# Performance work log

Measured on AMD Instinct MI355X. Metric: run time of the kernel, lower is better.

## Reference

```python
import jax, jax.numpy as jnp
import numpy as np

N_NODES = 100000

def _sage_conv(x, src, dst, deg_inv, Wl, bl, Wr):
    # PyG SAGEConv (aggr='mean', root_weight=True):
    #   out = lin_l(mean_{j in N(i)} x_j) + lin_r(x_i)
    msg = x[src]                                            # [E, d]
    agg = jax.ops.segment_sum(msg, dst, num_segments=N_NODES)  # [N, d]
    agg = agg * deg_inv                                     # mean (0 for isolated nodes)
    return agg @ Wl.T + bl + x @ Wr.T


def setup_inputs() -> dict:
    key = jax.random.key(0)
    ks = jax.random.split(key, 12)
    N, E, d_in, d_h, d_out = N_NODES, 1600000, 64, 64, 32
    x = jax.random.normal(ks[0], (N, d_in), dtype=jnp.float32)
    edge_index = jax.random.randint(ks[1], (2, E), 0, N, dtype=jnp.int64)

    def glorot(k, shape):
        fan_in = shape[1]
        return jax.random.normal(k, shape, dtype=jnp.float32) / np.sqrt(fan_in)

    return {
        "x": x,
        "edge_index": edge_index,
        "W1l": glorot(ks[2], (d_h, d_in)), "b1l": jnp.zeros((d_h,), jnp.float32), "W1r": glorot(ks[3], (d_h, d_in)),
        "W2l": glorot(ks[4], (d_h, d_h)),  "b2l": jnp.zeros((d_h,), jnp.float32), "W2r": glorot(ks[5], (d_h, d_h)),
        "W3l": glorot(ks[6], (d_h, d_h)),  "b3l": jnp.zeros((d_h,), jnp.float32), "W3r": glorot(ks[7], (d_h, d_h)),
        "Wfc": glorot(ks[8], (d_out, d_h)), "bfc": jnp.zeros((d_out,), jnp.float32),
    }


def reference(x, edge_index, W1l, b1l, W1r, W2l, b2l, W2r, W3l, b3l, W3r, Wfc, bfc):
    src, dst = edge_index[0], edge_index[1]
    # in-degree per destination node (shared by all three conv layers)
    ones = jnp.ones((src.shape[0],), x.dtype)
    deg = jax.ops.segment_sum(ones, dst, num_segments=N_NODES)
    deg_inv = (1.0 / jnp.maximum(deg, 1.0))[:, None]        # [N, 1]

    h = jax.nn.relu(_sage_conv(x, src, dst, deg_inv, W1l, b1l, W1r))
    # dropout(p=0.5) is identity in eval mode
    h = jax.nn.relu(_sage_conv(h, src, dst, deg_inv, W2l, b2l, W2r))
    h = jax.nn.relu(_sage_conv(h, src, dst, deg_inv, W3l, b3l, W3r))
    return h @ Wfc.T + bfc
```

## Files before the change

### kernel.cpp

```cpp
#include <hip/hip_runtime.h>
#include <hip/hip_fp16.h>

#define N_NODES 100000
#define D 64
#define BR 256
#define NB 391
#define ECH 2560
#define NROWPAD 100096
#define CSRCAP 6144

typedef _Float16 f16x8 __attribute__((ext_vector_type(8)));
typedef float f32x4 __attribute__((ext_vector_type(4)));

__device__ __forceinline__ float rlf(float v, int l) {
    union { float f; int i; } u;
    u.f = v;
    u.i = __builtin_amdgcn_readlane(u.i, l);
    return u.f;
}

__global__ __launch_bounds__(256) void k_prep(const float* __restrict__ Wl1, const float* __restrict__ Wr1,
                                              const float* __restrict__ Wl2, const float* __restrict__ Wr2,
                                              const float* __restrict__ Wl3, const float* __restrict__ Wr3,
                                              const float* __restrict__ Wfc,
                                              __half* __restrict__ Wf1, __half* __restrict__ Wf2,
                                              __half* __restrict__ Wf3, __half* __restrict__ Wffc,
                                              unsigned* __restrict__ x16, unsigned* __restrict__ H1,
                                              unsigned* __restrict__ H2,
                                              int* __restrict__ histT, int entries, int ntail,
                                              const float4* __restrict__ x, int n4) {
    int t = blockIdx.x * 256 + threadIdx.x;
    if (t >= 65536) {
        int i = t - 65536;
        if (i < n4) {
            float4 v = x[i];
            union { __half2 h[2]; uint2 u; } pk;
            pk.h[0] = __floats2half2_rn(v.x, v.y);
            pk.h[1] = __floats2half2_rn(v.z, v.w);
            ((uint2*)x16)[i] = pk.u;
        }
    } else if (t < 24576) {
        int layer = t / 8192;
        int r = t % 8192;
        int f = r >> 9, rem = r & 511;
        int lane = rem >> 3, i = rem & 7;
        int kt = f >> 2, nt = f & 3;
        int k = kt * 32 + (lane >> 4) * 8 + i;
        int o = nt * 16 + (lane & 15);
        const float* Wl = layer == 0 ? Wl1 : layer == 1 ? Wl2 : Wl3;
        const float* Wr = layer == 0 ? Wr1 : layer == 1 ? Wr2 : Wr3;
        float v = (k < 64) ? Wl[o * 64 + k] : Wr[o * 64 + (k - 64)];
        __half* Wf = layer == 0 ? Wf1 : layer == 1 ? Wf2 : Wf3;
        Wf[r] = __float2half(v);
    } else if (t < 26624) {
        int r = t - 24576;
        int f = r >> 9, rem = r & 511;
        int lane = rem >> 3, i = rem & 7;
        int kt = f >> 1, nt = f & 1;
        int k = kt * 32 + (lane >> 4) * 8 + i;
        int o = nt * 16 + (lane & 15);
        Wffc[r] = __float2half(Wfc[o * 64 + k]);
    } else if (t < 26720) {
        int z = t - 26624;
        unsigned* buf = (z >> 5) == 0 ? x16 : (z >> 5) == 1 ? H1 : H2;
        buf[(size_t)N_NODES * 32 + (z & 31)] = 0u;
    } else if (t >= 32768 && t < 32768 + ntail) {
        histT[entries + (t - 32768)] = 0;
    }
}


__global__ __launch_bounds__(512) void k_hist(const int* __restrict__ dst,
                                              int* __restrict__ histT,
                                              int E, int ga) {
    __shared__ int h[NB];
    int blk = blockIdx.x, tid = threadIdx.x;
    for (int i = tid; i < NB; i += 512) h[i] = 0;
    __syncthreads();
    int base = blk * ECH;
    int lim = E - base; if (lim > ECH) lim = ECH;
    for (int i = tid; i < lim; i += 512)
        atomicAdd(&h[dst[base + i] >> 8], 1);
    __syncthreads();
    for (int i = tid; i < NB; i += 512)
        histT[i * ga + blk] = h[i];
}

__global__ __launch_bounds__(256) void k_scan1(const int* __restrict__ cnt,
                                               int* __restrict__ part,
                                               int* __restrict__ bsums) {
    __shared__ int s[256];
    int tid = threadIdx.x;
    int i4 = blockIdx.x * 256 + tid;
    int4 v = reinterpret_cast<const int4*>(cnt)[i4];
    int tsum = v.x + v.y + v.z + v.w;
    s[tid] = tsum;
    __syncthreads();
    for (int off = 1; off < 256; off <<= 1) {
        int t = 0;
        if (tid >= off) t = s[tid - off];
        __syncthreads();
        if (tid >= off) s[tid] += t;
        __syncthreads();
    }
    int excl = tid ? s[tid - 1] : 0;
    if (tid == 255) bsums[blockIdx.x] = s[255];
    int4 o;
    o.x = excl;
    o.y = o.x + v.x;
    o.z = o.y + v.y;
    o.w = o.z + v.z;
    reinterpret_cast<int4*>(part)[i4] = o;
}

__global__ __launch_bounds__(256) void k_scan2(int* __restrict__ bsums, int nb,
                                               int* __restrict__ col) {
    __shared__ int s[256];
    int tid = threadIdx.x;
    if (tid < 8) col[tid] = N_NODES;
    int v = (tid < nb) ? bsums[tid] : 0;
    s[tid] = v;
    __syncthreads();
    for (int off = 1; off < 256; off <<= 1) {
        int t = 0;
        if (tid >= off) t = s[tid - off];
        __syncthreads();
        if (tid >= off) s[tid] += t;
        __syncthreads();
    }
    if (tid < nb) bsums[tid] = tid ? s[tid - 1] : 0;
}

__global__ __launch_bounds__(512) void k_part(const int* __restrict__ src,
                                              const int* __restrict__ dst,
                                              const int* __restrict__ offs,
                                              const int* __restrict__ bsums,
                                              int* __restrict__ bedge,
                                              int E, int ga) {
    __shared__ int o[NB];
    int blk = blockIdx.x, tid = threadIdx.x;
    for (int i = tid; i < NB; i += 512) {
        int ent = i * ga + blk;
        o[i] = offs[ent] + bsums[ent >> 10];
    }
    __syncthreads();
    int base = blk * ECH;
    int lim = E - base; if (lim > ECH) lim = ECH;
    for (int i = tid; i < lim; i += 512) {
        int e = base + i;
        int d = dst[e];
        int pos = atomicAdd(&o[d >> 8], 1);
        bedge[pos] = src[e] | ((d & 255) << 17);
    }
}

__global__ __launch_bounds__(512) void k_csr(const int* __restrict__ bedge,
                                             const int* __restrict__ offs,
                                             const int* __restrict__ bsums,
                                             int* __restrict__ col,
                                             int2* __restrict__ rp,
                                             float* __restrict__ deg_inv,
                                             int E, int ga) {
    __shared__ int ebuf[CSRCAP];
    __shared__ int lcnt[BR];
    __shared__ int stmp[BR];
    __shared__ int lcur[BR];
    int b = blockIdx.x, tid = threadIdx.x;
    int e0 = b * ga;
    int ebeg = offs[e0] + bsums[e0 >> 10];
    int eend = E;
    if (b + 1 < NB) {
        int e1 = (b + 1) * ga;
        eend = offs[e1] + bsums[e1 >> 10];
    }
    int cnt = eend - ebeg;
    int nbase = b * BR;
    int cbase = ebeg + b * (BR * 4) + 8;
    if (tid < 256) lcnt[tid] = 0;
    __syncthreads();
    for (int i = tid; i < cnt; i += 512) {
        int ed = bedge[ebeg + i];
        if (i < CSRCAP) ebuf[i] = ed;
        atomicAdd(&lcnt[ed >> 17], 1);
    }
    __syncthreads();
    int v = 0, pdeg = 0;
    if (tid < 256) {
        v = lcnt[tid];
        pdeg = (v + 3) & ~3;
        stmp[tid] = pdeg;
    }
    __syncthreads();
    for (int off = 1; off < 256; off <<= 1) {
        int t = 0;
        if (tid < 256 && tid >= off) t = stmp[tid - off];
        __syncthreads();
        if (tid < 256 && tid >= off) stmp[tid] += t;
        __syncthreads();
    }
    if (tid < 256) {
        int ex = tid ? stmp[tid - 1] : 0;
        int slot = cbase + ex;
        lcur[tid] = slot;
        int node = nbase + tid;
        if (node < N_NODES) {
            rp[node] = make_int2(slot, slot + pdeg);
            deg_inv[node] = 1.0f / (float)(v > 1 ? v : 1);
            for (int s2 = slot + v; s2 < slot + pdeg; ++s2) col[s2] = N_NODES;
        }
    }
    __syncthreads();
    for (int i = tid; i < cnt; i += 512) {
        int ed = (i < CSRCAP) ? ebuf[i] : bedge[ebeg + i];
        int pos = atomicAdd(&lcur[ed >> 17], 1);
        col[pos] = ed & 0x1FFFF;
    }
}


__device__ __forceinline__ void fused_core(const __half* __restrict__ Hin,
                                           const __half* __restrict__ Wf,
                                           const float* __restrict__ bias,
                                           const int2* __restrict__ rp,
                                           const int* __restrict__ col,
                                           const float* __restrict__ deg_inv, int n,
                                           __half (&lds)[16][72], int m0, int l,
                                           f32x4 (&acc)[4]) {
    int q = l >> 4, li = l & 15;
    int beg = 0, nq = 0;
    float dinv = 0.f;
    if (l < 16 && m0 + l < n) {
        int2 se = rp[m0 + l];
        beg = se.x;
        nq = (se.y - se.x) >> 2;
        dinv = deg_inv[m0 + l];
    }
    const uint2* x8 = (const uint2*)Hin;
    const int* cq = col + q;

#pragma unroll
    for (int g = 0; g < 4; ++g) {
        int b0 = __builtin_amdgcn_readlane(beg, 4 * g + 0);
        int b1 = __builtin_amdgcn_readlane(beg, 4 * g + 1);
        int b2 = __builtin_amdgcn_readlane(beg, 4 * g + 2);
        int b3 = __builtin_amdgcn_readlane(beg, 4 * g + 3);
        int c0 = __builtin_amdgcn_readlane(nq, 4 * g + 0);
        int c1 = __builtin_amdgcn_readlane(nq, 4 * g + 1);
        int c2 = __builtin_amdgcn_readlane(nq, 4 * g + 2);
        int c3 = __builtin_amdgcn_readlane(nq, 4 * g + 3);
        int qmax = max(max(c0, c1), max(c2, c3));
        __half2 s00 = __floats2half2_rn(0.f, 0.f), s01 = s00;
        __half2 s10 = s00, s11 = s00, s20 = s00, s21 = s00, s30 = s00, s31 = s00;
        for (int qq = 0; qq < qmax; qq += 4) {
            int a[16];
#pragma unroll
            for (int s = 0; s < 4; ++s) {
                int o = (qq + s) * 4;
                a[s * 4 + 0] = qq + s < c0 ? b0 + o : 0;
                a[s * 4 + 1] = qq + s < c1 ? b1 + o : 0;
                a[s * 4 + 2] = qq + s < c2 ? b2 + o : 0;
                a[s * 4 + 3] = qq + s < c3 ? b3 + o : 0;
            }
            int idx[16];
#pragma unroll
            for (int i = 0; i < 16; ++i) idx[i] = cq[a[i]];
            uint2 u[16];
#pragma unroll
            for (int i = 0; i < 16; ++i) u[i] = x8[(size_t)idx[i] * 16 + li];
            union { unsigned v; __half2 h; } w;
#pragma unroll
            for (int s = 0; s < 4; ++s) {
                w.v = u[s * 4 + 0].x; s00 = __hadd2(s00, w.h);
                w.v = u[s * 4 + 0].y; s01 = __hadd2(s01, w.h);
                w.v = u[s * 4 + 1].x; s10 = __hadd2(s10, w.h);
                w.v = u[s * 4 + 1].y; s11 = __hadd2(s11, w.h);
                w.v = u[s * 4 + 2].x; s20 = __hadd2(s20, w.h);
                w.v = u[s * 4 + 2].y; s21 = __hadd2(s21, w.h);
                w.v = u[s * 4 + 3].x; s30 = __hadd2(s30, w.h);
                w.v = u[s * 4 + 3].y; s31 = __hadd2(s31, w.h);
            }
        }
        union { __half2 h; int i; } t;
#pragma unroll
        for (int m = 16; m < 64; m <<= 1) {
            t.h = s00; t.i = __shfl_xor(t.i, m); s00 = __hadd2(s00, t.h);
            t.h = s01; t.i = __shfl_xor(t.i, m); s01 = __hadd2(s01, t.h);
            t.h = s10; t.i = __shfl_xor(t.i, m); s10 = __hadd2(s10, t.h);
            t.h = s11; t.i = __shfl_xor(t.i, m); s11 = __hadd2(s11, t.h);
            t.h = s20; t.i = __shfl_xor(t.i, m); s20 = __hadd2(s20, t.h);
            t.h = s21; t.i = __shfl_xor(t.i, m); s21 = __hadd2(s21, t.h);
            t.h = s30; t.i = __shfl_xor(t.i, m); s30 = __hadd2(s30, t.h);
            t.h = s31; t.i = __shfl_xor(t.i, m); s31 = __hadd2(s31, t.h);
        }
        float d0 = rlf(dinv, 4 * g + 0);
        float d1 = rlf(dinv, 4 * g + 1);
        float d2 = rlf(dinv, 4 * g + 2);
        float d3 = rlf(dinv, 4 * g + 3);
        if (l < 16) {
            union { __half2 h; unsigned v; } p0, p1;
            float2 f;
            uint2 ov;
            f = __half22float2(s00); p0.h = __floats2half2_rn(f.x * d0, f.y * d0);
            f = __half22float2(s01); p1.h = __floats2half2_rn(f.x * d0, f.y * d0);
            ov.x = p0.v; ov.y = p1.v;
            *(uint2*)&lds[4 * g + 0][li * 4] = ov;
            f = __half22float2(s10); p0.h = __floats2half2_rn(f.x * d1, f.y * d1);
            f = __half22float2(s11); p1.h = __floats2half2_rn(f.x * d1, f.y * d1);
            ov.x = p0.v; ov.y = p1.v;
            *(uint2*)&lds[4 * g + 1][li * 4] = ov;
            f = __half22float2(s20); p0.h = __floats2half2_rn(f.x * d2, f.y * d2);
            f = __half22float2(s21); p1.h = __floats2half2_rn(f.x * d2, f.y * d2);
            ov.x = p0.v; ov.y = p1.v;
            *(uint2*)&lds[4 * g + 2][li * 4] = ov;
            f = __half22float2(s30); p0.h = __floats2half2_rn(f.x * d3, f.y * d3);
            f = __half22float2(s31); p1.h = __floats2half2_rn(f.x * d3, f.y * d3);
            ov.x = p0.v; ov.y = p1.v;
            *(uint2*)&lds[4 * g + 3][li * 4] = ov;
        }
    }

    const f16x8* wf8 = (const f16x8*)Wf;
    f16x8 bf[4][4];
#pragma unroll
    for (int kt = 0; kt < 4; ++kt)
#pragma unroll
        for (int nt = 0; nt < 4; ++nt)
            bf[kt][nt] = wf8[(kt * 4 + nt) * 64 + l];
    int rowA = li;
#pragma unroll
    for (int nt = 0; nt < 4; ++nt) {
        float bs = bias[nt * 16 + rowA];
        acc[nt] = (f32x4){bs, bs, bs, bs};
    }
#pragma unroll
    for (int kt = 0; kt < 4; ++kt) {
        f16x8 a;
        if (kt < 2)
            a = *(const f16x8*)&lds[rowA][kt * 32 + q * 8];
        else
            a = *(const f16x8*)(Hin + (size_t)(m0 + rowA) * D + (kt - 2) * 32 + q * 8);
#pragma unroll
        for (int nt = 0; nt < 4; ++nt)
            acc[nt] = __builtin_amdgcn_mfma_f32_16x16x32_f16(a, bf[kt][nt], acc[nt], 0, 0, 0);
    }
}

__global__ __launch_bounds__(256) void k_fused(const __half* __restrict__ Hin,
                                               __half* __restrict__ Hout,
                                               const __half* __restrict__ Wf,
                                               const float* __restrict__ bias,
                                               const int2* __restrict__ rp,
                                               const int* __restrict__ col,
                                               const float* __restrict__ deg_inv, int n) {
    __shared__ __half lds[4][16][72];
    int l = threadIdx.x & 63;
    int wv = threadIdx.x >> 6;
    int m0 = blockIdx.x * 64 + wv * 16;
    f32x4 acc[4];
    fused_core(Hin, Wf, bias, rp, col, deg_inv, n, lds[wv], m0, l, acc);
    int q = l >> 4, rowA = l & 15;
#pragma unroll
    for (int nt = 0; nt < 4; ++nt)
#pragma unroll
        for (int qd = 0; qd < 4; ++qd) {
            int node = m0 + q * 4 + qd;
            float v = fmaxf(acc[nt][qd], 0.f);
            if (node < n)
                Hout[(size_t)node * D + nt * 16 + rowA] = __float2half(v);
        }
}

__global__ __launch_bounds__(256) void k_fused_fc(const __half* __restrict__ Hin,
                                                  float* __restrict__ out,
                                                  const __half* __restrict__ Wf,
                                                  const float* __restrict__ bias,
                                                  const __half* __restrict__ Wffc,
                                                  const float* __restrict__ bfc,
                                                  const int2* __restrict__ rp,
                                                  const int* __restrict__ col,
                                                  const float* __restrict__ deg_inv, int n) {
    __shared__ __half lds[4][16][72];
    int l = threadIdx.x & 63;
    int wv = threadIdx.x >> 6;
    int m0 = blockIdx.x * 64 + wv * 16;
    f32x4 acc[4];
    fused_core(Hin, Wf, bias, rp, col, deg_inv, n, lds[wv], m0, l, acc);
    int q = l >> 4, li = l & 15;

#pragma unroll
    for (int nt = 0; nt < 4; ++nt)
#pragma unroll
        for (int qd = 0; qd < 4; ++qd)
            lds[wv][q * 4 + qd][nt * 16 + li] = __float2half(fmaxf(acc[nt][qd], 0.f));

    const f16x8* wfc8 = (const f16x8*)Wffc;
    f16x8 bf2[2][2];
#pragma unroll
    for (int kt = 0; kt < 2; ++kt)
#pragma unroll
        for (int nt = 0; nt < 2; ++nt)
            bf2[kt][nt] = wfc8[(kt * 2 + nt) * 64 + l];
    f32x4 acc2[2];
#pragma unroll
    for (int nt = 0; nt < 2; ++nt) {
        float bs = bfc[nt * 16 + li];
        acc2[nt] = (f32x4){bs, bs, bs, bs};
    }
#pragma unroll
    for (int kt = 0; kt < 2; ++kt) {
        f16x8 a = *(const f16x8*)&lds[wv][li][kt * 32 + q * 8];
#pragma unroll
        for (int nt = 0; nt < 2; ++nt)
            acc2[nt] = __builtin_amdgcn_mfma_f32_16x16x32_f16(a, bf2[kt][nt], acc2[nt], 0, 0, 0);
    }
#pragma unroll
    for (int nt = 0; nt < 2; ++nt)
#pragma unroll
        for (int qd = 0; qd < 4; ++qd) {
            int node = m0 + q * 4 + qd;
            if (node < n)
                out[(size_t)node * 32 + nt * 16 + li] = acc2[nt][qd];
        }
}


extern "C" void kernel_launch(void* const* d_in, const int* in_sizes, int n_in,
                              void* d_out, int out_size, void* d_ws, size_t ws_size,
                              hipStream_t stream) {
    const float* x   = (const float*)d_in[0];
    const int*   ei  = (const int*)d_in[1];
    const int    E   = in_sizes[1] / 2;
    const int*   src = ei;
    const int*   dst = ei + E;
    const float* W1l = (const float*)d_in[2];
    const float* b1l = (const float*)d_in[3];
    const float* W1r = (const float*)d_in[4];
    const float* W2l = (const float*)d_in[5];
    const float* b2l = (const float*)d_in[6];
    const float* W2r = (const float*)d_in[7];
    const float* W3l = (const float*)d_in[8];
    const float* b3l = (const float*)d_in[9];
    const float* W3r = (const float*)d_in[10];
    const float* Wfc = (const float*)d_in[11];
    const float* bfc = (const float*)d_in[12];
    float* out = (float*)d_out;

    const int ga      = (E + ECH - 1) / ECH;
    const int entries = NB * ga;
    const int padded  = (entries + 1023) & ~1023;
    const int ntail   = padded - entries;
    const int nb2     = padded / 1024;

    char* p = (char*)d_ws;
    size_t off = 0;
    auto take = [&](size_t bytes) -> void* {
        void* r = p + off;
        off = (off + bytes + 255) & ~(size_t)255;
        return r;
    };
    __half* x16    = (__half*)take((size_t)NROWPAD * D * 2);
    __half* H1     = (__half*)take((size_t)NROWPAD * D * 2);
    __half* H2     = (__half*)take((size_t)NROWPAD * D * 2);
    float* deg_inv = (float*)take((size_t)N_NODES * 4);
    int2*  rp      = (int2*)take((size_t)N_NODES * 8);
    int*   histT   = (int*)take((size_t)padded * 4);
    int*   offs    = (int*)take((size_t)padded * 4);
    int*   bsums   = (int*)take(256 * 4);
    int*   bedge   = (int*)take((size_t)E * 4);
    int*   col     = (int*)take((size_t)(E + NB * BR * 4 + 72) * 4);
    __half* Wf1    = (__half*)take(8192 * 2);
    __half* Wf2    = (__half*)take(8192 * 2);
    __half* Wf3    = (__half*)take(8192 * 2);
    __half* Wffc   = (__half*)take(2048 * 2);

    int n4 = N_NODES * D / 4;
    int gp = (65536 + n4 + 255) / 256;
    k_prep<<<gp, 256, 0, stream>>>(W1l, W1r, W2l, W2r, W3l, W3r, Wfc,
                                   Wf1, Wf2, Wf3, Wffc,
                                   (unsigned*)x16, (unsigned*)H1, (unsigned*)H2,
                                   histT, entries, ntail, (const float4*)x, n4);

    k_hist<<<ga, 512, 0, stream>>>(dst, histT, E, ga);
    k_scan1<<<nb2, 256, 0, stream>>>(histT, offs, bsums);
    k_scan2<<<1, 256, 0, stream>>>(bsums, nb2, col);
    k_part<<<ga, 512, 0, stream>>>(src, dst, offs, bsums, bedge, E, ga);
    k_csr<<<NB, 512, 0, stream>>>(bedge, offs, bsums, col, rp, deg_inv, E, ga);

    int gg = NROWPAD / 64;

    k_fused<<<gg, 256, 0, stream>>>(x16, H1, Wf1, b1l, rp, col, deg_inv, N_NODES);
    k_fused<<<gg, 256, 0, stream>>>(H1, H2, Wf2, b2l, rp, col, deg_inv, N_NODES);
    k_fused_fc<<<gg, 256, 0, stream>>>(H2, out, Wf3, b3l, Wffc, bfc, rp, col, deg_inv, N_NODES);
}
```

Baseline: 182.8 us.

## Split features into column slices and separate aggregation from GEMM

Feature matrices move to a sliced layout: four 16-column fp16 slices, each stored contiguously across all nodes. Aggregation becomes its own kernel that gathers one slice at a time, aiming for better cache locality of random gathers since each slice is a quarter of the full matrix. A separate MFMA GEMM kernel then reads the aggregated and root slices. This doubles the kernel launches and adds a round trip of the aggregate buffer through global memory.

Measured after the change: 420.2 us. 130% more time.

```diff
diff --git a/kernel.cpp b/kernel.cpp
--- a/kernel.cpp
+++ b/kernel.cpp
@@ -7,17 +7,10 @@
 #define NB 391
 #define ECH 2560
 #define NROWPAD 100096
-#define CSRCAP 6144
+#define SS ((size_t)NROWPAD * 16)
 
 typedef _Float16 f16x8 __attribute__((ext_vector_type(8)));
 typedef float f32x4 __attribute__((ext_vector_type(4)));
-
-__device__ __forceinline__ float rlf(float v, int l) {
-    union { float f; int i; } u;
-    u.f = v;
-    u.i = __builtin_amdgcn_readlane(u.i, l);
-    return u.f;
-}
 
 __global__ __launch_bounds__(256) void k_prep(const float* __restrict__ Wl1, const float* __restrict__ Wr1,
                                               const float* __restrict__ Wl2, const float* __restrict__ Wr2,
@@ -25,19 +18,27 @@
                                               const float* __restrict__ Wfc,
                                               __half* __restrict__ Wf1, __half* __restrict__ Wf2,
                                               __half* __restrict__ Wf3, __half* __restrict__ Wffc,
-                                              unsigned* __restrict__ x16, unsigned* __restrict__ H1,
-                                              unsigned* __restrict__ H2,
+                                              __half* __restrict__ x16, __half* __restrict__ H1,
+                                              __half* __restrict__ H2,
                                               int* __restrict__ histT, int entries, int ntail,
-                                              const float4* __restrict__ x, int n4) {
+                                              const float* __restrict__ x, int ncv) {
     int t = blockIdx.x * 256 + threadIdx.x;
     if (t >= 65536) {
         int i = t - 65536;
-        if (i < n4) {
-            float4 v = x[i];
-            union { __half2 h[2]; uint2 u; } pk;
-            pk.h[0] = __floats2half2_rn(v.x, v.y);
-            pk.h[1] = __floats2half2_rn(v.z, v.w);
-            ((uint2*)x16)[i] = pk.u;
+        if (i < ncv) {
+            int nd = i >> 2, p = i & 3;
+            const float4* xp = (const float4*)x + (size_t)nd * 16 + p * 4;
+            float4 v0 = xp[0], v1 = xp[1], v2 = xp[2], v3 = xp[3];
+            union { __half2 h; unsigned u; } a, b;
+            __half* d = x16 + (size_t)p * SS + (size_t)nd * 16;
+            a.h = __floats2half2_rn(v0.x, v0.y); b.h = __floats2half2_rn(v0.z, v0.w);
+            ((uint2*)d)[0] = make_uint2(a.u, b.u);
+            a.h = __floats2half2_rn(v1.x, v1.y); b.h = __floats2half2_rn(v1.z, v1.w);
+            ((uint2*)d)[1] = make_uint2(a.u, b.u);
+            a.h = __floats2half2_rn(v2.x, v2.y); b.h = __floats2half2_rn(v2.z, v2.w);
+            ((uint2*)d)[2] = make_uint2(a.u, b.u);
+            a.h = __floats2half2_rn(v3.x, v3.y); b.h = __floats2half2_rn(v3.z, v3.w);
+            ((uint2*)d)[3] = make_uint2(a.u, b.u);
         }
     } else if (t < 24576) {
         int layer = t / 8192;
@@ -62,8 +63,10 @@
         Wffc[r] = __float2half(Wfc[o * 64 + k]);
     } else if (t < 26720) {
         int z = t - 26624;
-        unsigned* buf = (z >> 5) == 0 ? x16 : (z >> 5) == 1 ? H1 : H2;
-        buf[(size_t)N_NODES * 32 + (z & 31)] = 0u;
+        int bsel = z >> 5, rem = z & 31;
+        int s = rem >> 3, u = rem & 7;
+        __half* buf = bsel == 0 ? x16 : bsel == 1 ? H1 : H2;
+        ((unsigned*)buf)[(size_t)s * (SS / 2) + (size_t)N_NODES * 8 + u] = 0u;
     } else if (t >= 32768 && t < 32768 + ntail) {
         histT[entries + (t - 32768)] = 0;
     }
@@ -117,7 +120,7 @@
                                                int* __restrict__ col) {
     __shared__ int s[256];
     int tid = threadIdx.x;
-    if (tid < 8) col[tid] = N_NODES;
+    if (tid < 16) col[tid] = N_NODES;
     int v = (tid < nb) ? bsums[tid] : 0;
     s[tid] = v;
     __syncthreads();
@@ -154,6 +157,7 @@
     }
 }
 
+#define CSRCAP 6144
 __global__ __launch_bounds__(512) void k_csr(const int* __restrict__ bedge,
                                              const int* __restrict__ offs,
                                              const int* __restrict__ bsums,
@@ -175,7 +179,7 @@
     }
     int cnt = eend - ebeg;
     int nbase = b * BR;
-    int cbase = ebeg + b * (BR * 4) + 8;
+    int cbase = ebeg + b * (BR * 4) + 16;
     if (tid < 256) lcnt[tid] = 0;
     __syncthreads();
     for (int i = tid; i < cnt; i += 512) {
@@ -218,107 +222,66 @@
 }
 
 
-__device__ __forceinline__ void fused_core(const __half* __restrict__ Hin,
-                                           const __half* __restrict__ Wf,
-                                           const float* __restrict__ bias,
-                                           const int2* __restrict__ rp,
-                                           const int* __restrict__ col,
-                                           const float* __restrict__ deg_inv, int n,
-                                           __half (&lds)[16][72], int m0, int l,
-                                           f32x4 (&acc)[4]) {
-    int q = l >> 4, li = l & 15;
-    int beg = 0, nq = 0;
-    float dinv = 0.f;
-    if (l < 16 && m0 + l < n) {
-        int2 se = rp[m0 + l];
-        beg = se.x;
-        nq = (se.y - se.x) >> 2;
-        dinv = deg_inv[m0 + l];
-    }
-    const uint2* x8 = (const uint2*)Hin;
-    const int* cq = col + q;
-
-#pragma unroll
-    for (int g = 0; g < 4; ++g) {
-        int b0 = __builtin_amdgcn_readlane(beg, 4 * g + 0);
-        int b1 = __builtin_amdgcn_readlane(beg, 4 * g + 1);
-        int b2 = __builtin_amdgcn_readlane(beg, 4 * g + 2);
-        int b3 = __builtin_amdgcn_readlane(beg, 4 * g + 3);
-        int c0 = __builtin_amdgcn_readlane(nq, 4 * g + 0);
-        int c1 = __builtin_amdgcn_readlane(nq, 4 * g + 1);
-        int c2 = __builtin_amdgcn_readlane(nq, 4 * g + 2);
-        int c3 = __builtin_amdgcn_readlane(nq, 4 * g + 3);
-        int qmax = max(max(c0, c1), max(c2, c3));
-        __half2 s00 = __floats2half2_rn(0.f, 0.f), s01 = s00;
-        __half2 s10 = s00, s11 = s00, s20 = s00, s21 = s00, s30 = s00, s31 = s00;
-        for (int qq = 0; qq < qmax; qq += 4) {
-            int a[16];
-#pragma unroll
-            for (int s = 0; s < 4; ++s) {
-                int o = (qq + s) * 4;
-                a[s * 4 + 0] = qq + s < c0 ? b0 + o : 0;
-                a[s * 4 + 1] = qq + s < c1 ? b1 + o : 0;
-                a[s * 4 + 2] = qq + s < c2 ? b2 + o : 0;
-                a[s * 4 + 3] = qq + s < c3 ? b3 + o : 0;
-            }
-            int idx[16];
-#pragma unroll
-            for (int i = 0; i < 16; ++i) idx[i] = cq[a[i]];
-            uint2 u[16];
-#pragma unroll
-            for (int i = 0; i < 16; ++i) u[i] = x8[(size_t)idx[i] * 16 + li];
+__global__ __launch_bounds__(256) void k_aggslice(const __half* __restrict__ Hin,
+                                                  __half* __restrict__ Agg,
+                                                  const int2* __restrict__ rp,
+                                                  const int* __restrict__ col,
+                                                  const float* __restrict__ deg_inv,
+                                                  int bps, int n) {
+    int slice = blockIdx.x / bps;
+    int blk = blockIdx.x % bps;
+    int l = threadIdx.x & 63;
+    int wv = threadIdx.x >> 6;
+    int e4 = l >> 2, c = l & 3;
+    int nbase = (blk * 4 + wv) * 16;
+    const __half* src = Hin + (size_t)slice * SS;
+    __half* dst = Agg + (size_t)slice * SS;
+    for (int i = 0; i < 16; ++i) {
+        int node = nbase + i;
+        if (node >= n) break;
+        int2 se = rp[node];
+        int beg = __builtin_amdgcn_readfirstlane(se.x);
+        int pdeg = __builtin_amdgcn_readfirstlane(se.y) - beg;
+        __half2 a0 = __floats2half2_rn(0.f, 0.f), a1 = a0;
+        for (int base = 0; base < pdeg; base += 16) {
+            int e = base + e4;
+            int addr = e < pdeg ? beg + e : e4;
+            int idx = col[addr];
+            uint2 u = *(const uint2*)(src + (size_t)idx * 16 + c * 4);
             union { unsigned v; __half2 h; } w;
-#pragma unroll
-            for (int s = 0; s < 4; ++s) {
-                w.v = u[s * 4 + 0].x; s00 = __hadd2(s00, w.h);
-                w.v = u[s * 4 + 0].y; s01 = __hadd2(s01, w.h);
-                w.v = u[s * 4 + 1].x; s10 = __hadd2(s10, w.h);
-                w.v = u[s * 4 + 1].y; s11 = __hadd2(s11, w.h);
-                w.v = u[s * 4 + 2].x; s20 = __hadd2(s20, w.h);
-                w.v = u[s * 4 + 2].y; s21 = __hadd2(s21, w.h);
-                w.v = u[s * 4 + 3].x; s30 = __hadd2(s30, w.h);
-                w.v = u[s * 4 + 3].y; s31 = __hadd2(s31, w.h);
-            }
-        }
-        union { __half2 h; int i; } t;
-#pragma unroll
-        for (int m = 16; m < 64; m <<= 1) {
-            t.h = s00; t.i = __shfl_xor(t.i, m); s00 = __hadd2(s00, t.h);
-            t.h = s01; t.i = __shfl_xor(t.i, m); s01 = __hadd2(s01, t.h);
-            t.h = s10; t.i = __shfl_xor(t.i, m); s10 = __hadd2(s10, t.h);
-            t.h = s11; t.i = __shfl_xor(t.i, m); s11 = __hadd2(s11, t.h);
-            t.h = s20; t.i = __shfl_xor(t.i, m); s20 = __hadd2(s20, t.h);
-            t.h = s21; t.i = __shfl_xor(t.i, m); s21 = __hadd2(s21, t.h);
-            t.h = s30; t.i = __shfl_xor(t.i, m); s30 = __hadd2(s30, t.h);
-            t.h = s31; t.i = __shfl_xor(t.i, m); s31 = __hadd2(s31, t.h);
-        }
-        float d0 = rlf(dinv, 4 * g + 0);
-        float d1 = rlf(dinv, 4 * g + 1);
-        float d2 = rlf(dinv, 4 * g + 2);
-        float d3 = rlf(dinv, 4 * g + 3);
-        if (l < 16) {
+            w.v = u.x; a0 = __hadd2(a0, w.h);
+            w.v = u.y; a1 = __hadd2(a1, w.h);
+        }
+        union { __half2 h; int i2; } t0, t1;
+#pragma unroll
+        for (int m = 4; m < 64; m <<= 1) {
+            t0.h = a0; t0.i2 = __shfl_xor(t0.i2, m); a0 = __hadd2(a0, t0.h);
+            t1.h = a1; t1.i2 = __shfl_xor(t1.i2, m); a1 = __hadd2(a1, t1.h);
+        }
+        if (l < 4) {
+            float di = deg_inv[node];
+            float2 f0 = __half22float2(a0), f1 = __half22float2(a1);
             union { __half2 h; unsigned v; } p0, p1;
-            float2 f;
-            uint2 ov;
-            f = __half22float2(s00); p0.h = __floats2half2_rn(f.x * d0, f.y * d0);
-            f = __half22float2(s01); p1.h = __floats2half2_rn(f.x * d0, f.y * d0);
-            ov.x = p0.v; ov.y = p1.v;
-            *(uint2*)&lds[4 * g + 0][li * 4] = ov;
-            f = __half22float2(s10); p0.h = __floats2half2_rn(f.x * d1, f.y * d1);
-            f = __half22float2(s11); p1.h = __floats2half2_rn(f.x * d1, f.y * d1);
-            ov.x = p0.v; ov.y = p1.v;
-            *(uint2*)&lds[4 * g + 1][li * 4] = ov;
-            f = __half22float2(s20); p0.h = __floats2half2_rn(f.x * d2, f.y * d2);
-            f = __half22float2(s21); p1.h = __floats2half2_rn(f.x * d2, f.y * d2);
-            ov.x = p0.v; ov.y = p1.v;
-            *(uint2*)&lds[4 * g + 2][li * 4] = ov;
-            f = __half22float2(s30); p0.h = __floats2half2_rn(f.x * d3, f.y * d3);
-            f = __half22float2(s31); p1.h = __floats2half2_rn(f.x * d3, f.y * d3);
-            ov.x = p0.v; ov.y = p1.v;
-            *(uint2*)&lds[4 * g + 3][li * 4] = ov;
-        }
-    }
-
+            p0.h = __floats2half2_rn(f0.x * di, f0.y * di);
+            p1.h = __floats2half2_rn(f1.x * di, f1.y * di);
+            *(uint2*)(dst + (size_t)node * 16 + c * 4) = make_uint2(p0.v, p1.v);
+        }
+    }
+}
+
+
+template <bool FC>
+__global__ __launch_bounds__(256) void k_mgemm(const __half* __restrict__ Agg,
+                                               const __half* __restrict__ Hin,
+                                               const __half* __restrict__ Wf,
+                                               const float* __restrict__ bias,
+                                               const __half* __restrict__ Wffc,
+                                               const float* __restrict__ bfc,
+                                               void* __restrict__ outp, int n) {
+    int l = threadIdx.x & 63;
+    int wv = threadIdx.x >> 6;
+    int m0 = blockIdx.x * 64 + wv * 16;
+    int rowA = l & 15, q = l >> 4;
     const f16x8* wf8 = (const f16x8*)Wf;
     f16x8 bf[4][4];
 #pragma unroll
@@ -326,101 +289,71 @@
 #pragma unroll
         for (int nt = 0; nt < 4; ++nt)
             bf[kt][nt] = wf8[(kt * 4 + nt) * 64 + l];
-    int rowA = li;
+    f32x4 acc[4];
 #pragma unroll
     for (int nt = 0; nt < 4; ++nt) {
         float bs = bias[nt * 16 + rowA];
         acc[nt] = (f32x4){bs, bs, bs, bs};
     }
+    int sA = (q >> 1) * 1;
+    int offA = (q & 1) * 8;
 #pragma unroll
     for (int kt = 0; kt < 4; ++kt) {
-        f16x8 a;
-        if (kt < 2)
-            a = *(const f16x8*)&lds[rowA][kt * 32 + q * 8];
-        else
-            a = *(const f16x8*)(Hin + (size_t)(m0 + rowA) * D + (kt - 2) * 32 + q * 8);
+        const __half* sp = (kt < 2) ? Agg : Hin;
+        int sl = (kt & 1) * 2 + sA;
+        f16x8 a = *(const f16x8*)(sp + (size_t)sl * SS + (size_t)(m0 + rowA) * 16 + offA);
 #pragma unroll
         for (int nt = 0; nt < 4; ++nt)
             acc[nt] = __builtin_amdgcn_mfma_f32_16x16x32_f16(a, bf[kt][nt], acc[nt], 0, 0, 0);
     }
-}
-
-__global__ __launch_bounds__(256) void k_fused(const __half* __restrict__ Hin,
-                                               __half* __restrict__ Hout,
-                                               const __half* __restrict__ Wf,
-                                               const float* __restrict__ bias,
-                                               const int2* __restrict__ rp,
-                                               const int* __restrict__ col,
-                                               const float* __restrict__ deg_inv, int n) {
-    __shared__ __half lds[4][16][72];
-    int l = threadIdx.x & 63;
-    int wv = threadIdx.x >> 6;
-    int m0 = blockIdx.x * 64 + wv * 16;
-    f32x4 acc[4];
-    fused_core(Hin, Wf, bias, rp, col, deg_inv, n, lds[wv], m0, l, acc);
-    int q = l >> 4, rowA = l & 15;
-#pragma unroll
-    for (int nt = 0; nt < 4; ++nt)
-#pragma unroll
-        for (int qd = 0; qd < 4; ++qd) {
-            int node = m0 + q * 4 + qd;
-            float v = fmaxf(acc[nt][qd], 0.f);
-            if (node < n)
-                Hout[(size_t)node * D + nt * 16 + rowA] = __float2half(v);
-        }
-}
-
-__global__ __launch_bounds__(256) void k_fused_fc(const __half* __restrict__ Hin,
-                                                  float* __restrict__ out,
-                                                  const __half* __restrict__ Wf,
-                                                  const float* __restrict__ bias,
-                                                  const __half* __restrict__ Wffc,
-                                                  const float* __restrict__ bfc,
-                                                  const int2* __restrict__ rp,
-                                                  const int* __restrict__ col,
-                                                  const float* __restrict__ deg_inv, int n) {
-    __shared__ __half lds[4][16][72];
-    int l = threadIdx.x & 63;
-    int wv = threadIdx.x >> 6;
-    int m0 = blockIdx.x * 64 + wv * 16;
-    f32x4 acc[4];
-    fused_core(Hin, Wf, bias, rp, col, deg_inv, n, lds[wv], m0, l, acc);
-    int q = l >> 4, li = l & 15;
-
-#pragma unroll
-    for (int nt = 0; nt < 4; ++nt)
-#pragma unroll
-        for (int qd = 0; qd < 4; ++qd)
-            lds[wv][q * 4 + qd][nt * 16 + li] = __float2half(fmaxf(acc[nt][qd], 0.f));
-
-    const f16x8* wfc8 = (const f16x8*)Wffc;
-    f16x8 bf2[2][2];
-#pragma unroll
-    for (int kt = 0; kt < 2; ++kt)
+    if constexpr (!FC) {
+        __half* Hout = (__half*)outp;
+#pragma unroll
+        for (int nt = 0; nt < 4; ++nt)
+#pragma unroll
+            for (int qd = 0; qd < 4; ++qd) {
+                int node = m0 + q * 4 + qd;
+                float v = fmaxf(acc[nt][qd], 0.f);
+                if (node < n)
+                    Hout[(size_t)nt * SS + (size_t)node * 16 + rowA] = __float2half(v);
+            }
+    } else {
+        __shared__ __half lds[4][16][72];
+#pragma unroll
+        for (int nt = 0; nt < 4; ++nt)
+#pragma unroll
+            for (int qd = 0; qd < 4; ++qd)
+                lds[wv][q * 4 + qd][nt * 16 + rowA] = __float2half(fmaxf(acc[nt][qd], 0.f));
+        const f16x8* wfc8 = (const f16x8*)Wffc;
+        f16x8 bf2[2][2];
+#pragma unroll
+        for (int kt = 0; kt < 2; ++kt)
+#pragma unroll
+            for (int nt = 0; nt < 2; ++nt)
+                bf2[kt][nt] = wfc8[(kt * 2 + nt) * 64 + l];
+        f32x4 acc2[2];
+#pragma unroll
+        for (int nt = 0; nt < 2; ++nt) {
+            float bs = bfc[nt * 16 + rowA];
+            acc2[nt] = (f32x4){bs, bs, bs, bs};
+        }
+#pragma unroll
+        for (int kt = 0; kt < 2; ++kt) {
+            f16x8 a = *(const f16x8*)&lds[wv][rowA][kt * 32 + q * 8];
+#pragma unroll
+            for (int nt = 0; nt < 2; ++nt)
+                acc2[nt] = __builtin_amdgcn_mfma_f32_16x16x32_f16(a, bf2[kt][nt], acc2[nt], 0, 0, 0);
+        }
+        float* out = (float*)outp;
 #pragma unroll
         for (int nt = 0; nt < 2; ++nt)
-            bf2[kt][nt] = wfc8[(kt * 2 + nt) * 64 + l];
-    f32x4 acc2[2];
-#pragma unroll
-    for (int nt = 0; nt < 2; ++nt) {
-        float bs = bfc[nt * 16 + li];
-        acc2[nt] = (f32x4){bs, bs, bs, bs};
-    }
-#pragma unroll
-    for (int kt = 0; kt < 2; ++kt) {
-        f16x8 a = *(const f16x8*)&lds[wv][li][kt * 32 + q * 8];
-#pragma unroll
-        for (int nt = 0; nt < 2; ++nt)
-            acc2[nt] = __builtin_amdgcn_mfma_f32_16x16x32_f16(a, bf2[kt][nt], acc2[nt], 0, 0, 0);
-    }
-#pragma unroll
-    for (int nt = 0; nt < 2; ++nt)
-#pragma unroll
-        for (int qd = 0; qd < 4; ++qd) {
-            int node = m0 + q * 4 + qd;
-            if (node < n)
-                out[(size_t)node * 32 + nt * 16 + li] = acc2[nt][qd];
-        }
+#pragma unroll
+            for (int qd = 0; qd < 4; ++qd) {
+                int node = m0 + q * 4 + qd;
+                if (node < n)
+                    out[(size_t)node * 32 + nt * 16 + rowA] = acc2[nt][qd];
+            }
+    }
 }
 
 
@@ -458,27 +391,27 @@
         off = (off + bytes + 255) & ~(size_t)255;
         return r;
     };
-    __half* x16    = (__half*)take((size_t)NROWPAD * D * 2);
-    __half* H1     = (__half*)take((size_t)NROWPAD * D * 2);
-    __half* H2     = (__half*)take((size_t)NROWPAD * D * 2);
+    __half* x16    = (__half*)take(SS * 4 * 2);
+    __half* H1     = (__half*)take(SS * 4 * 2);
+    __half* H2     = (__half*)take(SS * 4 * 2);
+    __half* A      = (__half*)take(SS * 4 * 2);
     float* deg_inv = (float*)take((size_t)N_NODES * 4);
     int2*  rp      = (int2*)take((size_t)N_NODES * 8);
     int*   histT   = (int*)take((size_t)padded * 4);
     int*   offs    = (int*)take((size_t)padded * 4);
     int*   bsums   = (int*)take(256 * 4);
     int*   bedge   = (int*)take((size_t)E * 4);
-    int*   col     = (int*)take((size_t)(E + NB * BR * 4 + 72) * 4);
+    int*   col     = (int*)take((size_t)(E + NB * BR * 4 + 80) * 4);
     __half* Wf1    = (__half*)take(8192 * 2);
     __half* Wf2    = (__half*)take(8192 * 2);
     __half* Wf3    = (__half*)take(8192 * 2);
     __half* Wffc   = (__half*)take(2048 * 2);
 
-    int n4 = N_NODES * D / 4;
-    int gp = (65536 + n4 + 255) / 256;
+    int ncv = N_NODES * 4;
+    int gp = (65536 + ncv + 255) / 256;
     k_prep<<<gp, 256, 0, stream>>>(W1l, W1r, W2l, W2r, W3l, W3r, Wfc,
                                    Wf1, Wf2, Wf3, Wffc,
-                                   (unsigned*)x16, (unsigned*)H1, (unsigned*)H2,
-                                   histT, entries, ntail, (const float4*)x, n4);
+                                   x16, H1, H2, histT, entries, ntail, x, ncv);
 
     k_hist<<<ga, 512, 0, stream>>>(dst, histT, E, ga);
     k_scan1<<<nb2, 256, 0, stream>>>(histT, offs, bsums);
@@ -486,9 +419,14 @@
     k_part<<<ga, 512, 0, stream>>>(src, dst, offs, bsums, bedge, E, ga);
     k_csr<<<NB, 512, 0, stream>>>(bedge, offs, bsums, col, rp, deg_inv, E, ga);
 
-    int gg = NROWPAD / 64;
-
-    k_fused<<<gg, 256, 0, stream>>>(x16, H1, Wf1, b1l, rp, col, deg_inv, N_NODES);
-    k_fused<<<gg, 256, 0, stream>>>(H1, H2, Wf2, b2l, rp, col, deg_inv, N_NODES);
-    k_fused_fc<<<gg, 256, 0, stream>>>(H2, out, Wf3, b3l, Wffc, bfc, rp, col, deg_inv, N_NODES);
-}
+    int bps = (N_NODES + 63) / 64;
+    int gs  = 4 * bps;
+    int gg  = NROWPAD / 64;
+
+    k_aggslice<<<gs, 256, 0, stream>>>(x16, A, rp, col, deg_inv, bps, N_NODES);
+    k_mgemm<false><<<gg, 256, 0, stream>>>(A, x16, Wf1, b1l, nullptr, nullptr, H1, N_NODES);
+    k_aggslice<<<gs, 256, 0, stream>>>(H1, A, rp, col, deg_inv, bps, N_NODES);
+    k_mgemm<false><<<gg, 256, 0, stream>>>(A, H1, Wf2, b2l, nullptr, nullptr, H2, N_NODES);
+    k_aggslice<<<gs, 256, 0, stream>>>(H2, A, rp, col, deg_inv, bps, N_NODES);
+    k_mgemm<true><<<gg, 256, 0, stream>>>(A, H2, Wf3, b3l, Wffc, bfc, out, N_NODES);
+}
```
